# Kernel optimization log

Measured on AMD Instinct MI355X. Metric: run time of the kernel, lower is better.

The kernel has to match this reference:

```python
import jax, jax.numpy as jnp
import numpy as np
from jax.scipy.ndimage import map_coordinates

N = 512      # image H=W (x0.shape[2])
A = 30       # number of projection angles (sparse-view CT)
D = 729      # det_count (hardcoded in source)
L = 3        # LayerNo
B = 2        # batch
P = 2048     # FFT padding: next pow2 >= 2*D


def _ramp_filter(size):
    # standard Ram-Lak filter built in spatial domain (skimage/torch-radon style)
    n = np.concatenate((np.arange(1, size // 2 + 1, 2), np.arange(size // 2 - 1, 0, -2)))
    f = np.zeros(size)
    f[0] = 0.25
    f[1::2] = -1.0 / (np.pi * n) ** 2
    return jnp.asarray(2.0 * np.real(np.fft.fft(f))[: size // 2 + 1], dtype=jnp.float32)


def setup_inputs() -> dict:
    key = jax.random.key(0)
    ks = jax.random.split(key, 8)
    x0 = jax.random.normal(ks[0], (B, 1, N, N), jnp.float32)
    sinogram = jax.random.normal(ks[1], (B, 1, A, D), jnp.float32)
    theta = jnp.linspace(0.0, np.pi, A, endpoint=False).astype(jnp.float32)
    theta_label = theta
    # denoiser params, stacked over L unrolled layers
    w1 = jax.random.normal(ks[2], (L, 32, 1, 3, 3), jnp.float32) * 0.1
    b1 = jnp.zeros((L, 32), jnp.float32)
    w2 = jax.random.normal(ks[3], (L, 32, 32, 3, 3), jnp.float32) * 0.05
    b2 = jnp.zeros((L, 32), jnp.float32)
    w3 = jax.random.normal(ks[4], (L, 32, 32, 3, 3), jnp.float32) * 0.05
    b3 = jnp.zeros((L, 32), jnp.float32)
    w4 = jax.random.normal(ks[5], (L, 1, 32, 3, 3), jnp.float32) * 0.05
    steps = jnp.ones((L,), jnp.float32)  # step_n params (requires_grad=False)
    return {"cond": 1, "x0": x0, "sinogram": sinogram, "theta": theta,
            "theta_label": theta_label, "w1": w1, "b1": b1, "w2": w2, "b2": b2,
            "w3": w3, "b3": b3, "w4": w4, "steps": steps}


def _conv(x, w, b=None):
    y = jax.lax.conv_general_dilated(x, w, (1, 1), 'SAME',
                                     dimension_numbers=('NCHW', 'OIHW', 'NCHW'))
    return y if b is None else y + b[None, :, None, None]


def _denoiser(x, w1, b1, w2, b2, w3, b3, w4):
    h = jax.nn.relu(_conv(x, w1, b1))
    h = jax.nn.relu(_conv(h, w2, b2))
    h = jax.nn.relu(_conv(h, w3, b3))
    return _conv(h, w4)


def _geometry(theta):
    # parallel-beam ray sampling grid: rows/cols [A, D, T] with T=D samples (dt=1)
    c = (N - 1) / 2.0
    s = jnp.arange(D, dtype=jnp.float32) - (D - 1) / 2.0  # detector coords
    t = s                                                  # along-ray samples
    cs, sn = jnp.cos(theta), jnp.sin(theta)
    x = s[None, :, None] * cs[:, None, None] - t[None, None, :] * sn[:, None, None]
    y = s[None, :, None] * sn[:, None, None] + t[None, None, :] * cs[:, None, None]
    return y + c, x + c  # rows, cols


def _radon_fwd(imgs, rows, cols):
    # imgs [B,N,N] -> sinogram [B,A,D] via bilinear line-integral sampling
    sample = lambda im: map_coordinates(im, [rows, cols], order=1, mode='constant', cval=0.0)
    return jax.vmap(sample)(imgs).sum(-1)


def _filter_sino(sino, filt):
    F = jnp.fft.rfft(sino, n=P, axis=-1)
    g = jnp.fft.irfft(F * filt, n=P, axis=-1)[..., :D]
    return g * (jnp.pi / (2.0 * A))  # FBP normalization


def _backproj(sino, theta):
    # sino [B,A,D] -> image [B,N,N], linear interp along detector axis
    c = (N - 1) / 2.0
    xs = jnp.arange(N, dtype=jnp.float32) - c
    cs, sn = jnp.cos(theta), jnp.sin(theta)
    sgrid = cs[:, None, None] * xs[None, None, :] + sn[:, None, None] * xs[None, :, None]  # [A,N,N]
    idx = sgrid + (D - 1) / 2.0
    lo = jnp.floor(idx).astype(jnp.int32)
    w = idx - lo
    lo_ok = (lo >= 0) & (lo < D)
    hi_ok = (lo + 1 >= 0) & (lo + 1 < D)
    lo_c = jnp.clip(lo, 0, D - 1)
    hi_c = jnp.clip(lo + 1, 0, D - 1)
    a = jnp.arange(A)[:, None, None]
    v = sino[:, a, lo_c] * jnp.where(lo_ok, 1.0 - w, 0.0) + \
        sino[:, a, hi_c] * jnp.where(hi_ok, w, 0.0)       # [B,A,N,N]
    return v.sum(axis=1)


def reference(cond, x0, sinogram, theta, theta_label, w1, b1, w2, b2, w3, b3, w4, steps):
    rows, cols = _geometry(theta)
    filt = _ramp_filter(P)
    X = x0[:, 0]           # [B,N,N]
    sino = sinogram[:, 0]  # [B,A,D]
    for n in range(L):
        sino_pred = _radon_fwd(X, rows, cols)
        filtered = _filter_sino(sino_pred, filt)
        outputs = _backproj(sino - filtered, theta)
        z = X + steps[n] * outputs
        noise = _denoiser(X[:, None], w1[n], b1[n], w2[n], b2[n], w3[n], b3[n], w4[n])[:, 0]
        filtered_noise = _filter_sino(_radon_fwd(noise, rows, cols), filt)
        outputs_noise = _backproj(filtered_noise, theta)
        X = z + noise - steps[n] * outputs_noise
    Xo = X[:, None]
    return (Xo, Xo, Xo)
```

## Files before the change

### kernel.cpp

```cpp
#include <hip/hip_runtime.h>
#include <hip/hip_bf16.h>

typedef __hip_bfloat16 bf16;
typedef __attribute__((ext_vector_type(8))) short short8;
typedef __attribute__((ext_vector_type(4))) short s4v;
typedef __attribute__((ext_vector_type(4))) float float4v;

#define NN 512
#define NA 30
#define ND 729
#define NB 2
#define NL 3
#define BNN (NB*NN*NN)
#define BAD (NB*NA*ND)

#define PW 520
#define PH 516
#define PIMG (PH*PW)
#define POFF (2*PW + 2)

#define O_CS  0
#define O_SN  32
#define O_ICS 64
#define O_ISN 96
#define O_XP  128
#define O_YP  (O_XP + 2*PIMG)
#define O_SP  (O_YP + 2*PIMG)
#define O_Q   (O_SP + BAD)
#define O_WR  (O_Q + BAD)
#define O_H   (((O_WR + 34560) + 15) & ~15)
#define H_FLOATS (NB * 32 * NN * NN / 2)

#define WR2_OFF 0
#define WR3_OFF 27648
#define WR4_OFF 55296

__device__ __forceinline__ float2 ld2u(const float* p)
{
    float2 r;
    __builtin_memcpy(&r, p, 8);
    return r;
}

__global__ void k_prep(const float* __restrict__ theta,
                       const float* __restrict__ w2, const float* __restrict__ w3,
                       const float* __restrict__ w4, const float* __restrict__ x0,
                       float* __restrict__ ws, bf16* __restrict__ wr)
{
    int idx = blockIdx.x * 256 + threadIdx.x;
    if (idx < NA) {
        float t = theta[idx];
        float cs = cosf(t), sn = sinf(t);
        ws[O_CS + idx] = cs;
        ws[O_SN + idx] = sn;
        ws[O_ICS + idx] = 1.0f / cs;
        ws[O_ISN + idx] = -1.0f / sn;
    }
    if (idx < 2 * 27648) {
        const float* w = (idx < 27648) ? w2 : w3;
        int base = (idx < 27648) ? WR2_OFF : WR3_OFF;
        int r = idx % 27648;
        int n = r / 9216; int r2 = r % 9216;
        int tap = r2 / 1024; int r3 = r2 % 1024;
        int co = r3 / 32, ci = r3 % 32;
        wr[base + r] = __float2bfloat16(w[n * 9216 + (co * 32 + ci) * 9 + tap]);
    } else if (idx < 2 * 27648 + 3 * 4608) {
        int r = idx - 2 * 27648;
        int n = r / 4608; int r2 = r % 4608;
        int tap = r2 / 512; int r3 = r2 % 512;
        int co = r3 / 32, ci = r3 % 32;
        float v = (co == 0) ? w4[n * 288 + ci * 9 + tap] : 0.f;
        wr[WR4_OFF + r] = __float2bfloat16(v);
    }
    if (idx < 2 * PIMG) {
        int b = idx / PIMG, p = idx % PIMG;
        int y = p / PW, x = p % PW;
        bool interior = (y >= 2 && y < 2 + NN && x >= 2 && x < 2 + NN);
        float v = interior ? x0[b * NN * NN + (y - 2) * NN + (x - 2)] : 0.f;
        ws[O_XP + idx] = v;
        if (!interior) ws[O_YP + idx] = 0.f;
    }
}

__device__ __forceinline__ void isect2(float A, float inv, float lo, float hi,
                                       float& tlo, float& thi)
{
    float a = (lo - A) * inv, b = (hi - A) * inv;
    tlo = fmaxf(tlo, fminf(a, b));
    thi = fminf(thi, fmaxf(a, b));
}

__global__ __launch_bounds__(256) void k_radon(const float* __restrict__ img,
    const float* __restrict__ ws, float* __restrict__ out)
{
    int b = blockIdx.z, a = blockIdx.y;
    int wave = threadIdx.x >> 6;
    int lane = threadIdx.x & 63;
    int s = blockIdx.x * 4 + wave;
    if (s >= ND) return;
    float cs = ws[O_CS + a], sn = ws[O_SN + a];
    float ics = ws[O_ICS + a], isn = ws[O_ISN + a];
    float s_c = (float)s - 364.0f;
    float A_r = 255.5f + s_c * sn;
    float A_c = 255.5f + s_c * cs;

    float tlo = -1e9f, thi = 1e9f;
    isect2(A_r, ics, -1.0f, 512.0f, tlo, thi);
    isect2(A_c, isn, -1.0f, 512.0f, tlo, thi);
    float t0f = fmaxf(tlo + 364.0f, 0.0f);
    float t1f = fminf(thi + 364.0f, 728.0f);

    float acc = 0.f;
    if (t0f <= t1f) {
        int tb = (int)ceilf(t0f);
        int te = (int)floorf(t1f);
        const float* im = img + b * PIMG;
#pragma unroll 2
        for (int t = tb + lane; t <= te; t += 64) {
            float tc = (float)t - 364.0f;
            float r = fmaf(tc, cs, A_r);
            float c = fmaf(-tc, sn, A_c);
            float rf = floorf(r), cf = floorf(c);
            float dr = r - rf, dc = c - cf;
            int idx = (int)rf * PW + (int)cf;
            float2 tp = ld2u(im + idx);
            float2 bt = ld2u(im + idx + PW);
            float top = fmaf(dc, tp.y - tp.x, tp.x);
            float bot = fmaf(dc, bt.y - bt.x, bt.x);
            acc = fmaf(dr, bot - top, acc + top);
        }
    }
    acc += __shfl_down(acc, 32, 64);
    acc += __shfl_down(acc, 16, 64);
    acc += __shfl_down(acc, 8, 64);
    acc += __shfl_down(acc, 4, 64);
    acc += __shfl_down(acc, 2, 64);
    acc += __shfl_down(acc, 1, 64);
    if (lane == 0) out[(b * NA + a) * ND + s] = acc;
}

__global__ void k_filter(const float* __restrict__ sp, const float* __restrict__ sino,
                         float* __restrict__ q)
{
    __shared__ float row[ND];
    __shared__ float taps[364];
    int ba = blockIdx.y;
    const float* src = sp + ba * ND;
    for (int i = threadIdx.x; i < ND; i += 256) row[i] = src[i];
    const float PI2 = 9.86960440108936f;
    for (int i = threadIdx.x; i < 364; i += 256) {
        float m = (float)(2 * i + 1);
        taps[i] = -2.0f / (PI2 * m * m);
    }
    __syncthreads();
    const float scale = 0.0523598775598299f;
    int d = blockIdx.x * 256 + threadIdx.x;
    if (d < ND) {
        float g0 = 0.5f * row[d], g1 = 0.f;
#pragma unroll 4
        for (int j = 0; j < 364; j += 2) {
            int m0 = 2 * j + 1, m1 = 2 * j + 3;
            float l0 = (d - m0 >= 0) ? row[d - m0] : 0.f;
            float r0 = (d + m0 < ND) ? row[d + m0] : 0.f;
            g0 = fmaf(taps[j], l0 + r0, g0);
            float l1 = (d - m1 >= 0) ? row[d - m1] : 0.f;
            float r1 = (d + m1 < ND) ? row[d + m1] : 0.f;
            g1 = fmaf(taps[j + 1], l1 + r1, g1);
        }
        q[ba * ND + d] = sino[ba * ND + d] - scale * (g0 + g1);
    }
}

__global__ __launch_bounds__(256) void k_backproj_update(const float* __restrict__ q,
    const float* __restrict__ src1, const float* __restrict__ ws,
    const float* __restrict__ steps, int n, float* __restrict__ out,
    float* __restrict__ outcopy)
{
    __shared__ float qt[NA][28];
    __shared__ int dmin_s[NA];
    int b = blockIdx.z;
    int x0 = blockIdx.x * 16, y0 = blockIdx.y * 16;
    int tid = threadIdx.x;
    int lx = tid & 15, ly = tid >> 4;
    const float* qb = q + b * NA * ND;

    for (int idx = tid; idx < NA * 26; idx += 256) {
        int a = idx / 26, j = idx % 26;
        float cs = ws[O_CS + a], sn = ws[O_SN + a];
        float f00 = fmaf(cs, (float)x0 - 255.5f, fmaf(sn, (float)y0 - 255.5f, 364.0f));
        float fmn = f00 + fminf(cs * 15.f, 0.f) + fminf(sn * 15.f, 0.f);
        int dm = (int)floorf(fmn);
        if (j == 0) dmin_s[a] = dm;
        int d = dm + j;
        qt[a][j] = (d >= 0 && d < ND) ? qb[a * ND + d] : 0.f;
    }
    __syncthreads();

    float xc = (float)(x0 + lx) - 255.5f, yc = (float)(y0 + ly) - 255.5f;
    float acc = 0.f;
#pragma unroll
    for (int a = 0; a < NA; a++) {
        float cs = ws[O_CS + a], sn = ws[O_SN + a];
        float f = fmaf(cs, xc, fmaf(sn, yc, 364.0f));
        float lf = floorf(f);
        float w = f - lf;
        int j = (int)lf - dmin_s[a];
        float v0 = qt[a][j], v1 = qt[a][j + 1];
        acc = fmaf(v0, 1.0f - w, fmaf(v1, w, acc));
    }
    int pidx = b * PIMG + (y0 + ly) * PW + (x0 + lx);
    float v = fmaf(steps[n], acc, src1[pidx]);
    out[pidx] = v;
    if (outcopy) {
        int fidx = b * NN * NN + (y0 + ly) * NN + (x0 + lx);
        outcopy[fidx] = v;
        outcopy[fidx + BNN] = v;
        outcopy[fidx + 2 * BNN] = v;
    }
}

__global__ __launch_bounds__(256) void k_conv1_hwc(const float* __restrict__ inb,
    const float* __restrict__ W, const float* __restrict__ B, bf16* __restrict__ outb)
{
    int bz = blockIdx.y;
    const float* in = inb + bz * PIMG;
    bf16* out = outb + (size_t)bz * NN * NN * 32;
    int idx = blockIdx.x * 256 + threadIdx.x;
    int y = idx >> 9, x = idx & (NN - 1);
    float v[9];
#pragma unroll
    for (int dy = 0; dy < 3; dy++)
#pragma unroll
        for (int dx = 0; dx < 3; dx++)
            v[dy * 3 + dx] = in[(y + dy - 1) * PW + (x + dx - 1)];
#pragma unroll
    for (int g = 0; g < 4; g++) {
        short8 pk;
#pragma unroll
        for (int j = 0; j < 8; j++) {
            int co = g * 8 + j;
            float a = B[co];
            const float* w = W + co * 9;
#pragma unroll
            for (int k = 0; k < 9; k++) a = fmaf(v[k], w[k], a);
            a = fmaxf(a, 0.f);
            bf16 h = __float2bfloat16(a);
            pk[j] = *reinterpret_cast<short*>(&h);
        }
        *(short8*)(out + (size_t)idx * 32 + g * 8) = pk;
    }
}

#define SH 8
template<int NCO, bool RELU, bool HASB, bool OUTF32>
__global__ __launch_bounds__(256) void k_conv_stream(const bf16* __restrict__ inb,
    const bf16* __restrict__ Wr, const float* __restrict__ Bs,
    const float* __restrict__ addsrc, void* __restrict__ outv)
{
    int lane = threadIdx.x & 63;
    int wave = threadIdx.x >> 6;
    int n16 = lane & 15, quad = lane >> 4;
    int b = blockIdx.z;
    int x0 = blockIdx.x * 16;
    int y0 = (blockIdx.y * 4 + wave) * SH;
    const bf16* in = inb + (size_t)b * NN * NN * 32;

    short8 wf[9 * NCO];
#pragma unroll
    for (int tap = 0; tap < 9; tap++)
#pragma unroll
        for (int t = 0; t < NCO; t++)
            wf[tap * NCO + t] = *(const short8*)(Wr + ((tap * NCO + t) * 16 + n16) * 32 + quad * 8);

    bool vx[3];
#pragma unroll
    for (int dx = 0; dx < 3; dx++) {
        int xx = x0 + n16 + dx - 1;
        vx[dx] = (xx >= 0) && (xx < NN);
    }

    short8 win[3][3];
    auto loadrow = [&](int yy, short8* dst) {
        if (yy >= 0 && yy < NN) {
            const bf16* rowp = in + (size_t)yy * NN * 32;
#pragma unroll
            for (int dx = 0; dx < 3; dx++) {
                short8 v = {};
                if (vx[dx]) v = *(const short8*)(rowp + (x0 + n16 + dx - 1) * 32 + quad * 8);
                dst[dx] = v;
            }
        } else {
            dst[0] = short8{}; dst[1] = short8{}; dst[2] = short8{};
        }
    };
    loadrow(y0 - 1, win[0]);
    loadrow(y0,     win[1]);

    float4v bias[NCO];
#pragma unroll
    for (int t = 0; t < NCO; t++)
        bias[t] = HASB ? *(const float4v*)(Bs + t * 16 + quad * 4) : (float4v){0.f, 0.f, 0.f, 0.f};

#pragma unroll
    for (int i = 0; i < SH; i++) {
        int y = y0 + i;
        loadrow(y + 1, win[(i + 2) % 3]);
        float4v acc[NCO];
#pragma unroll
        for (int t = 0; t < NCO; t++) acc[t] = bias[t];
#pragma unroll
        for (int dy = 0; dy < 3; dy++) {
            short8* row = win[(i + dy) % 3];
#pragma unroll
            for (int dx = 0; dx < 3; dx++) {
                int tap = dy * 3 + dx;
#pragma unroll
                for (int t = 0; t < NCO; t++)
                    acc[t] = __builtin_amdgcn_mfma_f32_16x16x32_bf16(wf[tap * NCO + t], row[dx], acc[t], 0, 0, 0);
            }
        }
        if (OUTF32) {
            float* out = (float*)outv + b * PIMG;
            if (quad == 0) {
                int pi = y * PW + x0 + n16;
                out[pi] = addsrc[b * PIMG + pi] + acc[0][0];
            }
        } else {
            bf16* out = (bf16*)outv + (size_t)b * NN * NN * 32;
            bf16* pp = out + ((size_t)y * NN + x0 + n16) * 32 + quad * 4;
#pragma unroll
            for (int t = 0; t < NCO; t++) {
                s4v pk;
#pragma unroll
                for (int r = 0; r < 4; r++) {
                    float v = acc[t][r];
                    if (RELU) v = fmaxf(v, 0.f);
                    bf16 h = __float2bfloat16(v);
                    pk[r] = *reinterpret_cast<short*>(&h);
                }
                *(s4v*)(pp + t * 16) = pk;
            }
        }
    }
}

extern "C" void kernel_launch(void* const* d_in, const int* in_sizes, int n_in,
                              void* d_out, int out_size, void* d_ws, size_t ws_size,
                              hipStream_t stream)
{
    const float* x0    = (const float*)d_in[1];
    const float* sg    = (const float*)d_in[2];
    const float* theta = (const float*)d_in[3];
    const float* w1    = (const float*)d_in[5];
    const float* b1    = (const float*)d_in[6];
    const float* w2    = (const float*)d_in[7];
    const float* b2    = (const float*)d_in[8];
    const float* w3    = (const float*)d_in[9];
    const float* b3    = (const float*)d_in[10];
    const float* w4    = (const float*)d_in[11];
    const float* steps = (const float*)d_in[12];

    float* ws = (float*)d_ws;
    float* XP = ws + O_XP + POFF;
    float* YP = ws + O_YP + POFF;
    float* SP = ws + O_SP;
    float* Q  = ws + O_Q;
    bf16* wr  = (bf16*)(ws + O_WR);
    bf16* h1  = (bf16*)(ws + O_H);
    bf16* h2  = (bf16*)(ws + O_H + H_FLOATS);

    k_prep<<<(2 * PIMG + 255) / 256, 256, 0, stream>>>(theta, w2, w3, w4, x0, ws, wr);

    for (int n = 0; n < NL; n++) {
        k_conv1_hwc<<<dim3(NN * NN / 256, NB), 256, 0, stream>>>(XP, w1 + n * 288, b1 + n * 32, h1);
        k_conv_stream<2, true, true, false><<<dim3(32, 16, NB), 256, 0, stream>>>(
            h1, wr + WR2_OFF + n * 9216, b2 + n * 32, nullptr, h2);
        k_conv_stream<2, true, true, false><<<dim3(32, 16, NB), 256, 0, stream>>>(
            h2, wr + WR3_OFF + n * 9216, b3 + n * 32, nullptr, h1);
        k_conv_stream<1, false, false, true><<<dim3(32, 16, NB), 256, 0, stream>>>(
            h1, wr + WR4_OFF + n * 4608, nullptr, XP, YP);

        k_radon<<<dim3((ND + 3) / 4, NA, NB), 256, 0, stream>>>(YP, ws, SP);
        k_filter<<<dim3(3, NB * NA), 256, 0, stream>>>(SP, sg, Q);
        k_backproj_update<<<dim3(32, 32, NB), 256, 0, stream>>>(
            Q, YP, ws, steps, n, XP, (n == NL - 1) ? (float*)d_out : nullptr);
    }
}
```

Baseline: 471.8 us.

## Fuse conv1 into conv2 via shared-memory halo tile of first-layer activations

Replaces the separate first-conv kernel and the first MFMA conv kernel with one fused kernel. Each block computes the 32-channel conv1 output for a 34x18 halo tile into LDS in bf16, then runs the 3x3 32->32 MFMA convolution from LDS and writes h2. This removes the global write and reread of the full h1 activation tensor and one launch per layer. In exchange it recomputes conv1 on the halo region and adds LDS traffic and a block barrier.

```diff
diff --git a/kernel.cpp b/kernel.cpp
--- a/kernel.cpp
+++ b/kernel.cpp
@@ -219,35 +219,109 @@
     }
 }
 
-__global__ __launch_bounds__(256) void k_conv1_hwc(const float* __restrict__ inb,
-    const float* __restrict__ W, const float* __restrict__ B, bf16* __restrict__ outb)
-{
-    int bz = blockIdx.y;
-    const float* in = inb + bz * PIMG;
-    bf16* out = outb + (size_t)bz * NN * NN * 32;
-    int idx = blockIdx.x * 256 + threadIdx.x;
-    int y = idx >> 9, x = idx & (NN - 1);
-    float v[9];
-#pragma unroll
-    for (int dy = 0; dy < 3; dy++)
+__global__ __launch_bounds__(256) void k_conv12(const float* __restrict__ XPb,
+    const float* __restrict__ W1, const float* __restrict__ B1,
+    const bf16* __restrict__ Wr2, const float* __restrict__ B2,
+    bf16* __restrict__ outb)
+{
+    __shared__ bf16 h1t[34][18][32];
+    int b = blockIdx.z;
+    int x0 = blockIdx.x * 16;
+    int Y0 = blockIdx.y * 32;
+    const float* in = XPb + b * PIMG;
+
+    for (int p = threadIdx.x; p < 34 * 18; p += 256) {
+        int yy = p / 18, xx = p % 18;
+        int gy = Y0 + yy - 1, gx = x0 + xx - 1;
+        if (gy < 0 || gy >= NN || gx < 0 || gx >= NN) {
+#pragma unroll
+            for (int g = 0; g < 4; g++)
+                *(short8*)(&h1t[yy][xx][g * 8]) = short8{};
+        } else {
+            float v[9];
+#pragma unroll
+            for (int dy = 0; dy < 3; dy++)
+#pragma unroll
+                for (int dx = 0; dx < 3; dx++)
+                    v[dy * 3 + dx] = in[(gy + dy - 1) * PW + (gx + dx - 1)];
+#pragma unroll
+            for (int g = 0; g < 4; g++) {
+                short8 pk;
+#pragma unroll
+                for (int j = 0; j < 8; j++) {
+                    int co = g * 8 + j;
+                    float a = B1[co];
+                    const float* w = W1 + co * 9;
+#pragma unroll
+                    for (int k = 0; k < 9; k++) a = fmaf(v[k], w[k], a);
+                    a = fmaxf(a, 0.f);
+                    bf16 h = __float2bfloat16(a);
+                    pk[j] = *reinterpret_cast<short*>(&h);
+                }
+                *(short8*)(&h1t[yy][xx][g * 8]) = pk;
+            }
+        }
+    }
+    __syncthreads();
+
+    int lane = threadIdx.x & 63;
+    int wave = threadIdx.x >> 6;
+    int n16 = lane & 15, quad = lane >> 4;
+    int y0w = Y0 + wave * 8;
+
+    short8 wf[18];
+#pragma unroll
+    for (int tap = 0; tap < 9; tap++)
+#pragma unroll
+        for (int t = 0; t < 2; t++)
+            wf[tap * 2 + t] = *(const short8*)(Wr2 + ((tap * 2 + t) * 16 + n16) * 32 + quad * 8);
+
+    short8 win[3][3];
+    auto loadrow = [&](int yy, short8* dst) {
+        int ly = yy - (Y0 - 1);
 #pragma unroll
         for (int dx = 0; dx < 3; dx++)
-            v[dy * 3 + dx] = in[(y + dy - 1) * PW + (x + dx - 1)];
-#pragma unroll
-    for (int g = 0; g < 4; g++) {
-        short8 pk;
-#pragma unroll
-        for (int j = 0; j < 8; j++) {
-            int co = g * 8 + j;
-            float a = B[co];
-            const float* w = W + co * 9;
-#pragma unroll
-            for (int k = 0; k < 9; k++) a = fmaf(v[k], w[k], a);
-            a = fmaxf(a, 0.f);
-            bf16 h = __float2bfloat16(a);
-            pk[j] = *reinterpret_cast<short*>(&h);
-        }
-        *(short8*)(out + (size_t)idx * 32 + g * 8) = pk;
+            dst[dx] = *(const short8*)(&h1t[ly][n16 + dx][quad * 8]);
+    };
+    loadrow(y0w - 1, win[0]);
+    loadrow(y0w,     win[1]);
+
+    float4v bias[2];
+#pragma unroll
+    for (int t = 0; t < 2; t++)
+        bias[t] = *(const float4v*)(B2 + t * 16 + quad * 4);
+
+    bf16* out = outb + (size_t)b * NN * NN * 32;
+#pragma unroll
+    for (int i = 0; i < 8; i++) {
+        int y = y0w + i;
+        loadrow(y + 1, win[(i + 2) % 3]);
+        float4v acc[2];
+#pragma unroll
+        for (int t = 0; t < 2; t++) acc[t] = bias[t];
+#pragma unroll
+        for (int dy = 0; dy < 3; dy++) {
+            short8* row = win[(i + dy) % 3];
+#pragma unroll
+            for (int dx = 0; dx < 3; dx++) {
+                int tap = dy * 3 + dx;
+#pragma unroll
+                for (int t = 0; t < 2; t++)
+                    acc[t] = __builtin_amdgcn_mfma_f32_16x16x32_bf16(wf[tap * 2 + t], row[dx], acc[t], 0, 0, 0);
+            }
+        }
+        bf16* pp = out + ((size_t)y * NN + x0 + n16) * 32 + quad * 4;
+#pragma unroll
+        for (int t = 0; t < 2; t++) {
+            s4v pk;
+#pragma unroll
+            for (int r = 0; r < 4; r++) {
+                float v = fmaxf(acc[t][r], 0.f);
+                bf16 h = __float2bfloat16(v);
+                pk[r] = *reinterpret_cast<short*>(&h);
+            }
+            *(s4v*)(pp + t * 16) = pk;
+        }
     }
 }
 
@@ -372,9 +446,8 @@
     k_prep<<<(2 * PIMG + 255) / 256, 256, 0, stream>>>(theta, w2, w3, w4, x0, ws, wr);
 
     for (int n = 0; n < NL; n++) {
-        k_conv1_hwc<<<dim3(NN * NN / 256, NB), 256, 0, stream>>>(XP, w1 + n * 288, b1 + n * 32, h1);
-        k_conv_stream<2, true, true, false><<<dim3(32, 16, NB), 256, 0, stream>>>(
-            h1, wr + WR2_OFF + n * 9216, b2 + n * 32, nullptr, h2);
+        k_conv12<<<dim3(32, 16, NB), 256, 0, stream>>>(
+            XP, w1 + n * 288, b1 + n * 32, wr + WR2_OFF + n * 9216, b2 + n * 32, h2);
         k_conv_stream<2, true, true, false><<<dim3(32, 16, NB), 256, 0, stream>>>(
             h2, wr + WR3_OFF + n * 9216, b3 + n * 32, nullptr, h1);
         k_conv_stream<1, false, false, true><<<dim3(32, 16, NB), 256, 0, stream>>>(
```

After: 431.8 us. -8.5%, faster.
